# Performance work log

Measured on AMD Instinct MI355X. Metric: run time of the kernel, lower is better.

## Reference

```python
import jax, jax.numpy as jnp
import numpy as np

N, E, F_IN, HID, HEADS, NCLS = 50000, 800000, 512, 64, 4, 40
NEG_SLOPE = 0.2


def setup_inputs() -> dict:
    key = jax.random.key(0)
    ks = jax.random.split(key, 12)
    x = jax.random.normal(ks[0], (N, F_IN), jnp.float32)
    edge_index = jax.random.randint(ks[1], (2, E), 0, N, jnp.int32)
    edge_weight = jnp.ones((E,), jnp.float32)
    s1 = 1.0 / np.sqrt(F_IN)
    s2 = 1.0 / np.sqrt(HID * HEADS)
    return {
        "x": x,
        "edge_index": edge_index,
        "edge_weight": edge_weight,
        "W1": jax.random.normal(ks[2], (F_IN, HEADS * HID), jnp.float32) * s1,
        "a_src1": jax.random.normal(ks[3], (HEADS, HID), jnp.float32) * s1,
        "a_dst1": jax.random.normal(ks[4], (HEADS, HID), jnp.float32) * s1,
        "b1": jnp.zeros((HEADS * HID,), jnp.float32),
        "W2": jax.random.normal(ks[5], (HEADS * HID, NCLS), jnp.float32) * s2,
        "a_src2": jax.random.normal(ks[6], (1, NCLS), jnp.float32) * s2,
        "a_dst2": jax.random.normal(ks[7], (1, NCLS), jnp.float32) * s2,
        "b2": jnp.zeros((NCLS,), jnp.float32),
    }


def _gat_layer(x, src, dst, ew, W, a_s, a_d, b, heads, n):
    c = W.shape[1] // heads
    h = (x @ W).reshape(n, heads, c)                      # [N,H,C]
    alpha_s = jnp.einsum('nhc,hc->nh', h, a_s)            # [N,H]
    alpha_d = jnp.einsum('nhc,hc->nh', h, a_d)
    e = jax.nn.leaky_relu(alpha_s[src] + alpha_d[dst], NEG_SLOPE)  # [Et,H]
    # segment softmax over destination nodes (self-loops guarantee nonempty segs)
    m = jax.ops.segment_max(e, dst, num_segments=n)
    ex = jnp.exp(e - m[dst])
    denom = jax.ops.segment_sum(ex, dst, num_segments=n)
    alpha = ex / (denom[dst] + 1e-16)                     # [Et,H]
    alpha = alpha * ew[:, None]
    msg = h[src] * alpha[:, :, None]                      # [Et,H,C]
    out = jax.ops.segment_sum(msg, dst, num_segments=n)   # [N,H,C]
    return out.reshape(n, heads * c) + b


def reference(x, edge_index, edge_weight, W1, a_src1, a_dst1, b1, W2, a_src2, a_dst2, b2):
    n = x.shape[0]
    loop = jnp.arange(n, dtype=edge_index.dtype)
    src = jnp.concatenate([edge_index[0], loop])
    dst = jnp.concatenate([edge_index[1], loop])
    ew = jnp.concatenate([edge_weight, jnp.ones((n,), edge_weight.dtype)])
    h = _gat_layer(x, src, dst, ew, W1, a_src1, a_dst1, b1, HEADS, n)
    h = jax.nn.relu(h)  # dropout p=0.0, eval mode: no-op
    out = _gat_layer(h, src, dst, ew, W2, a_src2, a_dst2, b2, 1, n)
    return out  # Identity (log_softmax_return=False)
```

## Files before the change

kernel.cpp:

```cpp
#include <hip/hip_runtime.h>
#include <math.h>

#define N_NODES 50000
#define N_EDGES 800000
#define ET (N_EDGES + N_NODES)
#define F_IN 512
#define HID 64
#define HEADS 4
#define C1 (HEADS * HID)
#define NCLS 40
#define NEG_SLOPE 0.2f
#define NCHUNK ((N_NODES + 255) / 256)

#define BUK_SHIFT 9
#define BUK_NODES (1 << BUK_SHIFT)
#define NBUK ((N_NODES + BUK_NODES - 1) / BUK_NODES)
#define BFILL_STRIDE 32

typedef __attribute__((ext_vector_type(8))) short short8;
typedef __attribute__((ext_vector_type(4))) float floatx4;

__device__ __forceinline__ float leaky(float x) { return fmaxf(x, NEG_SLOPE * x); }

__device__ __forceinline__ unsigned short f2bf(float f) {
    unsigned u = __float_as_uint(f);
    u += 0x7fffu + ((u >> 16) & 1u);
    return (unsigned short)(u >> 16);
}
__device__ __forceinline__ float bf2f(unsigned short u) {
    return __uint_as_float(((unsigned)u) << 16);
}

__device__ __forceinline__ void edge_sd(int e, const int* __restrict__ ei,
                                        const float* __restrict__ ew,
                                        int& s, int& d, float& w) {
    if (e < N_EDGES) { s = ei[e]; d = ei[N_EDGES + e]; w = ew[e]; }
    else             { s = d = e - N_EDGES; w = 1.f; }
}

__global__ void hist_kernel(const int* __restrict__ ei, int* __restrict__ cnt) {
    int e = blockIdx.x * blockDim.x + threadIdx.x;
    if (e >= ET) return;
    int d = (e < N_EDGES) ? ei[N_EDGES + e] : e - N_EDGES;
    atomicAdd(&cnt[d], 1);
}

__global__ void chunk_sum_kernel(const int* __restrict__ cnt, int* __restrict__ sums) {
    __shared__ int sm[256];
    int i = blockIdx.x * 256 + threadIdx.x;
    sm[threadIdx.x] = (i < N_NODES) ? cnt[i] : 0;
    __syncthreads();
    for (int s = 128; s > 0; s >>= 1) {
        if (threadIdx.x < s) sm[threadIdx.x] += sm[threadIdx.x + s];
        __syncthreads();
    }
    if (threadIdx.x == 0) sums[blockIdx.x] = sm[0];
}

__global__ void scan_sums_kernel(int* __restrict__ sums) {
    __shared__ int sm[256];
    int i = threadIdx.x;
    int v = (i < NCHUNK) ? sums[i] : 0;
    sm[i] = v;
    __syncthreads();
    #pragma unroll
    for (int s = 1; s < 256; s <<= 1) {
        int t = (i >= s) ? sm[i - s] : 0;
        __syncthreads();
        sm[i] += t;
        __syncthreads();
    }
    if (i < NCHUNK) sums[i] = sm[i] - v;
}

__global__ void rowptr_kernel(const int* __restrict__ cnt, const int* __restrict__ sums,
                              int* __restrict__ row_ptr) {
    __shared__ int sm[256];
    int i = blockIdx.x * 256 + threadIdx.x;
    int v = (i < N_NODES) ? cnt[i] : 0;
    sm[threadIdx.x] = v;
    __syncthreads();
    #pragma unroll
    for (int s = 1; s < 256; s <<= 1) {
        int t = (threadIdx.x >= s) ? sm[threadIdx.x - s] : 0;
        __syncthreads();
        sm[threadIdx.x] += t;
        __syncthreads();
    }
    int excl = sm[threadIdx.x] - v + sums[blockIdx.x];
    if (i < N_NODES) row_ptr[i] = excl;
}

__global__ void bucket_init_kernel(const int* __restrict__ row_ptr, int* __restrict__ bfill) {
    int t = threadIdx.x;
    if (t < NBUK) bfill[t * BFILL_STRIDE] = row_ptr[t << BUK_SHIFT];
}

__global__ __launch_bounds__(256) void bucket_scatter_kernel(const int* __restrict__ ei,
                                                             const float* __restrict__ ew,
                                                             int* __restrict__ bfill,
                                                             int2* __restrict__ SB) {
    __shared__ int lcnt[NBUK];
    __shared__ int lbase[NBUK];
    int e = blockIdx.x * 256 + threadIdx.x;
    for (int i = threadIdx.x; i < NBUK; i += 256) lcnt[i] = 0;
    __syncthreads();
    int s = 0, d = 0, b = 0, rank = 0; float w = 0.f;
    bool valid = e < ET;
    if (valid) {
        edge_sd(e, ei, ew, s, d, w);
        b = d >> BUK_SHIFT;
        rank = atomicAdd(&lcnt[b], 1);
    }
    __syncthreads();
    for (int i = threadIdx.x; i < NBUK; i += 256) {
        int c = lcnt[i];
        lbase[i] = c ? atomicAdd(&bfill[i * BFILL_STRIDE], c) : 0;
    }
    __syncthreads();
    if (valid)
        SB[lbase[b] + rank] = make_int2(s | (d << 16), __float_as_int(w));
}

__global__ __launch_bounds__(512) void place_kernel(const int* __restrict__ row_ptr,
                                                    const int2* __restrict__ SB,
                                                    int2* __restrict__ E2) {
    __shared__ int lfill[BUK_NODES];
    int b = blockIdx.x;
    int n0 = b << BUK_SHIFT;
    int t = threadIdx.x;
    int node = n0 + t;
    lfill[t] = (node < N_NODES) ? row_ptr[node] : 0;
    __syncthreads();
    int beg = row_ptr[n0];
    int end = (b == NBUK - 1) ? ET : row_ptr[n0 + BUK_NODES];
    for (int i = beg + t; i < end; i += 512) {
        int2 rec = SB[i];
        int d = ((unsigned)rec.x) >> 16;
        int pos = atomicAdd(&lfill[d - n0], 1);
        E2[pos] = make_int2(rec.x & 0xffff, rec.y);
    }
}

__global__ void wt_prep_kernel(const float* __restrict__ W, unsigned short* __restrict__ WT) {
    __shared__ float tile[32][33];
    int k0 = blockIdx.x * 32;
    int n0 = blockIdx.y * 32;
    int tx = threadIdx.x, ty = threadIdx.y;
    #pragma unroll
    for (int i = 0; i < 32; i += 8)
        tile[ty + i][tx] = W[(size_t)(k0 + ty + i) * C1 + n0 + tx];
    __syncthreads();
    #pragma unroll
    for (int i = 0; i < 32; i += 8)
        WT[(size_t)(n0 + ty + i) * F_IN + k0 + tx] = f2bf(tile[tx][ty + i]);
}

__global__ __launch_bounds__(512) void gemm1_mfma_kernel(const float* __restrict__ X,
                                                         const unsigned short* __restrict__ WT,
                                                         const float* __restrict__ a_s1,
                                                         const float* __restrict__ a_d1,
                                                         unsigned short* __restrict__ H,
                                                         float* __restrict__ AS,
                                                         float* __restrict__ AD) {
    __shared__ short As[128][40];
    __shared__ short Bs[256][40];
    const int t = threadIdx.x;
    const int m0 = blockIdx.x * 128;
    const int lane = t & 63;
    const int wave = t >> 6;
    const int wm = wave >> 2;
    const int wn = wave & 3;
    const int l15 = lane & 15;
    const int quad = lane >> 4;

    const int ar = t >> 2;
    const int ac0 = (t & 3) * 8;
    const int gr = m0 + ar;
    const int bn = t >> 1;
    const int bc0 = (t & 1) * 16;

    floatx4 acc[4][4];
    #pragma unroll
    for (int i = 0; i < 4; i++)
        #pragma unroll
        for (int j = 0; j < 4; j++) acc[i][j] = (floatx4){0.f, 0.f, 0.f, 0.f};

    for (int k0 = 0; k0 < F_IN; k0 += 32) {
        float xv[8];
        if (gr < N_NODES) {
            const float4* p = (const float4*)(X + (size_t)gr * F_IN + k0 + ac0);
            float4 v0 = p[0], v1 = p[1];
            xv[0] = v0.x; xv[1] = v0.y; xv[2] = v0.z; xv[3] = v0.w;
            xv[4] = v1.x; xv[5] = v1.y; xv[6] = v1.z; xv[7] = v1.w;
        } else {
            #pragma unroll
            for (int i = 0; i < 8; i++) xv[i] = 0.f;
        }
        short8 av;
        #pragma unroll
        for (int i = 0; i < 8; i++) av[i] = (short)f2bf(xv[i]);
        *(short8*)&As[ar][ac0] = av;

        const short8* q = (const short8*)(WT + (size_t)bn * F_IN + k0 + bc0);
        *(short8*)&Bs[bn][bc0]     = q[0];
        *(short8*)&Bs[bn][bc0 + 8] = q[1];
        __syncthreads();

        short8 a[4], b[4];
        #pragma unroll
        for (int i = 0; i < 4; i++)
            a[i] = *(const short8*)&As[wm * 64 + i * 16 + l15][quad * 8];
        #pragma unroll
        for (int j = 0; j < 4; j++)
            b[j] = *(const short8*)&Bs[wn * 64 + j * 16 + l15][quad * 8];
        #pragma unroll
        for (int i = 0; i < 4; i++)
            #pragma unroll
            for (int j = 0; j < 4; j++)
                acc[i][j] = __builtin_amdgcn_mfma_f32_16x16x32_bf16(a[i], b[j], acc[i][j], 0, 0, 0);
        __syncthreads();
    }

    float asr[4], adr[4];
    #pragma unroll
    for (int j = 0; j < 4; j++) {
        asr[j] = a_s1[wn * HID + j * 16 + l15];
        adr[j] = a_d1[wn * HID + j * 16 + l15];
    }

    #pragma unroll
    for (int i = 0; i < 4; i++) {
        int rbase = m0 + wm * 64 + i * 16 + quad * 4;
        #pragma unroll
        for (int j = 0; j < 4; j++) {
            int col = wn * 64 + j * 16 + l15;
            #pragma unroll
            for (int r = 0; r < 4; r++) {
                int row = rbase + r;
                if (row < N_NODES) H[(size_t)row * C1 + col] = f2bf(acc[i][j][r]);
            }
        }
        #pragma unroll
        for (int r = 0; r < 4; r++) {
            int row = rbase + r;
            float s_ = acc[i][0][r] * asr[0] + acc[i][1][r] * asr[1]
                     + acc[i][2][r] * asr[2] + acc[i][3][r] * asr[3];
            float d_ = acc[i][0][r] * adr[0] + acc[i][1][r] * adr[1]
                     + acc[i][2][r] * adr[2] + acc[i][3][r] * adr[3];
            #pragma unroll
            for (int m = 8; m; m >>= 1) { s_ += __shfl_xor(s_, m); d_ += __shfl_xor(d_, m); }
            if (l15 == 0 && row < N_NODES) {
                AS[row * 4 + wn] = s_;
                AD[row * 4 + wn] = d_;
            }
        }
    }
}

__global__ __launch_bounds__(256) void agg1_csr_kernel(const int* __restrict__ row_ptr,
                                                       const int2* __restrict__ E2,
                                                       const float* __restrict__ AS,
                                                       const float* __restrict__ AD,
                                                       const unsigned short* __restrict__ H,
                                                       const float* __restrict__ b1,
                                                       unsigned short* __restrict__ OUT) {
    int n = blockIdx.x * 4 + (threadIdx.x >> 6);
    int lane = threadIdx.x & 63;
    if (n >= N_NODES) return;
    int l15 = lane & 15;
    int h = lane >> 4;
    int c0 = lane * 4;
    int beg = row_ptr[n];
    int end = (n + 1 < N_NODES) ? row_ptr[n + 1] : ET;
    float ad = AD[n * 4 + h];
    float den = 0.f;
    float a0 = 0.f, a1 = 0.f, a2 = 0.f, a3 = 0.f;

    for (int base = beg; base < end; base += 16) {
        int m = end - base; if (m > 16) m = 16;
        float pw = 0.f; int s = 0;
        if (l15 < m) {
            int2 e = E2[base + l15];
            s = e.x;
            float pe = __expf(leaky(AS[e.x * 4 + h] + ad));
            den += pe;
            pw = pe * __int_as_float(e.y);
        }
        int p = 0;
        for (; p + 4 <= m; p += 4) {
            int s0 = __shfl(s, p);
            int s1 = __shfl(s, p + 1);
            int s2 = __shfl(s, p + 2);
            int s3 = __shfl(s, p + 3);
            uint2 u0 = *(const uint2*)(H + (size_t)s0 * C1 + c0);
            uint2 u1 = *(const uint2*)(H + (size_t)s1 * C1 + c0);
            uint2 u2 = *(const uint2*)(H + (size_t)s2 * C1 + c0);
            uint2 u3 = *(const uint2*)(H + (size_t)s3 * C1 + c0);
            float w0 = __shfl(pw, h * 16 + p);
            float w1 = __shfl(pw, h * 16 + p + 1);
            float w2 = __shfl(pw, h * 16 + p + 2);
            float w3 = __shfl(pw, h * 16 + p + 3);
            a0 += w0 * __uint_as_float(u0.x << 16)         + w1 * __uint_as_float(u1.x << 16)
                + w2 * __uint_as_float(u2.x << 16)         + w3 * __uint_as_float(u3.x << 16);
            a1 += w0 * __uint_as_float(u0.x & 0xffff0000u) + w1 * __uint_as_float(u1.x & 0xffff0000u)
                + w2 * __uint_as_float(u2.x & 0xffff0000u) + w3 * __uint_as_float(u3.x & 0xffff0000u);
            a2 += w0 * __uint_as_float(u0.y << 16)         + w1 * __uint_as_float(u1.y << 16)
                + w2 * __uint_as_float(u2.y << 16)         + w3 * __uint_as_float(u3.y << 16);
            a3 += w0 * __uint_as_float(u0.y & 0xffff0000u) + w1 * __uint_as_float(u1.y & 0xffff0000u)
                + w2 * __uint_as_float(u2.y & 0xffff0000u) + w3 * __uint_as_float(u3.y & 0xffff0000u);
        }
        for (; p < m; p++) {
            int s0 = __shfl(s, p);
            uint2 u0 = *(const uint2*)(H + (size_t)s0 * C1 + c0);
            float w0 = __shfl(pw, h * 16 + p);
            a0 += w0 * __uint_as_float(u0.x << 16);
            a1 += w0 * __uint_as_float(u0.x & 0xffff0000u);
            a2 += w0 * __uint_as_float(u0.y << 16);
            a3 += w0 * __uint_as_float(u0.y & 0xffff0000u);
        }
    }
    den += __shfl_xor(den, 1);
    den += __shfl_xor(den, 2);
    den += __shfl_xor(den, 4);
    den += __shfl_xor(den, 8);

    float r = 1.f / (den + 1e-16f);
    float4 bv = *(const float4*)(b1 + c0);
    float v0 = a0 * r + bv.x, v1 = a1 * r + bv.y, v2 = a2 * r + bv.z, v3 = a3 * r + bv.w;
    v0 = v0 > 0.f ? v0 : 0.f;
    v1 = v1 > 0.f ? v1 : 0.f;
    v2 = v2 > 0.f ? v2 : 0.f;
    v3 = v3 > 0.f ? v3 : 0.f;
    uint2 o;
    o.x = ((unsigned)f2bf(v1) << 16) | (unsigned)f2bf(v0);
    o.y = ((unsigned)f2bf(v3) << 16) | (unsigned)f2bf(v2);
    *(uint2*)(OUT + (size_t)n * C1 + c0) = o;
}

#define BROW 264
__global__ __launch_bounds__(512) void gemm2_mfma_kernel(const unsigned short* __restrict__ A,
                                                         const float* __restrict__ W2,
                                                         const float* __restrict__ a_s2,
                                                         const float* __restrict__ a_d2,
                                                         unsigned short* __restrict__ H2b,
                                                         float* __restrict__ AS2,
                                                         float* __restrict__ AD2) {
    __shared__ short As[256][40];
    __shared__ short Bs[48 * BROW];
    const int t = threadIdx.x;
    const int m0 = blockIdx.x * 256;
    const int lane = t & 63;
    const int wave = t >> 6;
    const int l15 = lane & 15;
    const int quad = lane >> 4;

    for (int i = t; i < 48 * 256; i += 512) {
        int n = i >> 8, k = i & 255;
        float v = (n < NCLS) ? W2[k * NCLS + n] : 0.f;
        Bs[n * BROW + k] = (short)f2bf(v);
    }

    const int ar = t >> 1;
    const int ac0 = (t & 1) * 16;

    floatx4 acc[2][3];
    #pragma unroll
    for (int i = 0; i < 2; i++)
        #pragma unroll
        for (int j = 0; j < 3; j++) acc[i][j] = (floatx4){0.f, 0.f, 0.f, 0.f};

    for (int k0 = 0; k0 < C1; k0 += 32) {
        const short8* q = (const short8*)(A + (size_t)(m0 + ar) * C1 + k0 + ac0);
        short8 v0 = q[0], v1 = q[1];
        __syncthreads();
        *(short8*)&As[ar][ac0]     = v0;
        *(short8*)&As[ar][ac0 + 8] = v1;
        __syncthreads();

        short8 a[2], b[3];
        #pragma unroll
        for (int i = 0; i < 2; i++)
            a[i] = *(const short8*)&As[wave * 32 + i * 16 + l15][quad * 8];
        #pragma unroll
        for (int j = 0; j < 3; j++)
            b[j] = *(const short8*)&Bs[(j * 16 + l15) * BROW + k0 + quad * 8];
        #pragma unroll
        for (int i = 0; i < 2; i++)
            #pragma unroll
            for (int j = 0; j < 3; j++)
                acc[i][j] = __builtin_amdgcn_mfma_f32_16x16x32_bf16(a[i], b[j], acc[i][j], 0, 0, 0);
    }

    float asr[3], adr[3];
    #pragma unroll
    for (int j = 0; j < 3; j++) {
        int col = j * 16 + l15;
        asr[j] = (col < NCLS) ? a_s2[col] : 0.f;
        adr[j] = (col < NCLS) ? a_d2[col] : 0.f;
    }

    #pragma unroll
    for (int i = 0; i < 2; i++) {
        #pragma unroll
        for (int r = 0; r < 4; r++) {
            int row = m0 + wave * 32 + i * 16 + quad * 4 + r;
            float s_ = acc[i][0][r] * asr[0] + acc[i][1][r] * asr[1] + acc[i][2][r] * asr[2];
            float d_ = acc[i][0][r] * adr[0] + acc[i][1][r] * adr[1] + acc[i][2][r] * adr[2];
            #pragma unroll
            for (int m = 8; m; m >>= 1) { s_ += __shfl_xor(s_, m); d_ += __shfl_xor(d_, m); }
            if (l15 == 0 && row < N_NODES) { AS2[row] = s_; AD2[row] = d_; }
            #pragma unroll
            for (int j = 0; j < 3; j++) {
                int col = j * 16 + l15;
                if (col < NCLS && row < N_NODES)
                    H2b[(size_t)row * NCLS + col] = f2bf(acc[i][j][r]);
            }
        }
    }
}

__global__ __launch_bounds__(256) void agg2_csr_kernel(const int* __restrict__ row_ptr,
                                                       const int2* __restrict__ E2,
                                                       const float* __restrict__ AS,
                                                       const float* __restrict__ AD,
                                                       const unsigned short* __restrict__ H2b,
                                                       const float* __restrict__ b2,
                                                       float* __restrict__ OUT) {
    int lane = threadIdx.x & 63;
    int n = blockIdx.x * 4 + (threadIdx.x >> 6);
    if (n >= N_NODES) return;
    int beg = row_ptr[n];
    int end = (n + 1 < N_NODES) ? row_ptr[n + 1] : ET;
    float ad = AD[n];
    bool act = lane < NCLS;
    float den = 0.f, acc = 0.f;

    for (int base = beg; base < end; base += 64) {
        int m = end - base; if (m > 64) m = 64;
        float pw = 0.f; int s = 0;
        if (lane < m) {
            int2 e = E2[base + lane];
            s = e.x;
            float pe = __expf(leaky(AS[e.x] + ad));
            den += pe;
            pw = pe * __int_as_float(e.y);
        }
        int p = 0;
        for (; p + 4 <= m; p += 4) {
            int s0 = __shfl(s, p);
            int s1 = __shfl(s, p + 1);
            int s2 = __shfl(s, p + 2);
            int s3 = __shfl(s, p + 3);
            float w0 = __shfl(pw, p);
            float w1 = __shfl(pw, p + 1);
            float w2 = __shfl(pw, p + 2);
            float w3 = __shfl(pw, p + 3);
            if (act) {
                float h0 = bf2f(H2b[(size_t)s0 * NCLS + lane]);
                float h1 = bf2f(H2b[(size_t)s1 * NCLS + lane]);
                float h2 = bf2f(H2b[(size_t)s2 * NCLS + lane]);
                float h3 = bf2f(H2b[(size_t)s3 * NCLS + lane]);
                acc += w0 * h0 + w1 * h1 + w2 * h2 + w3 * h3;
            }
        }
        for (; p < m; p++) {
            int s0 = __shfl(s, p);
            float w0 = __shfl(pw, p);
            if (act) acc += w0 * bf2f(H2b[(size_t)s0 * NCLS + lane]);
        }
    }
    den += __shfl_xor(den, 1);
    den += __shfl_xor(den, 2);
    den += __shfl_xor(den, 4);
    den += __shfl_xor(den, 8);
    den += __shfl_xor(den, 16);
    den += __shfl_xor(den, 32);
    if (act) {
        float r = 1.f / (den + 1e-16f);
        OUT[(size_t)n * NCLS + lane] = acc * r + b2[lane];
    }
}

extern "C" void kernel_launch(void* const* d_in, const int* in_sizes, int n_in,
                              void* d_out, int out_size, void* d_ws, size_t ws_size,
                              hipStream_t stream) {
    const float* x    = (const float*)d_in[0];
    const int*   ei   = (const int*)d_in[1];
    const float* ew   = (const float*)d_in[2];
    const float* W1   = (const float*)d_in[3];
    const float* a_s1 = (const float*)d_in[4];
    const float* a_d1 = (const float*)d_in[5];
    const float* b1   = (const float*)d_in[6];
    const float* W2   = (const float*)d_in[7];
    const float* a_s2 = (const float*)d_in[8];
    const float* a_d2 = (const float*)d_in[9];
    const float* b2   = (const float*)d_in[10];
    float* out = (float*)d_out;

    unsigned short* H1b  = (unsigned short*)d_ws;
    unsigned short* OUT1b = H1b + (size_t)N_NODES * C1;
    float* AS1  = (float*)(OUT1b + (size_t)N_NODES * C1);
    float* AD1  = AS1 + N_NODES * HEADS;
    int* row_ptr = (int*)(AD1 + N_NODES * HEADS);
    int* cnt  = row_ptr + N_NODES;
    int* bfill = cnt + N_NODES;
    int2* E2  = (int2*)(bfill + N_NODES);
    int* sums = (int*)(E2 + ET);
    unsigned short* WT = (unsigned short*)(sums + NCHUNK);
    unsigned short* H2b = H1b;
    float* AS2  = (float*)(H2b + (size_t)N_NODES * NCLS);
    float* AD2  = AS2 + N_NODES;
    int2* SB = (int2*)H1b;

    hipMemsetAsync(cnt, 0, N_NODES * sizeof(int), stream);
    wt_prep_kernel<<<dim3(F_IN / 32, C1 / 32), dim3(32, 8), 0, stream>>>(W1, WT);
    hist_kernel<<<(ET + 255) / 256, 256, 0, stream>>>(ei, cnt);
    chunk_sum_kernel<<<NCHUNK, 256, 0, stream>>>(cnt, sums);
    scan_sums_kernel<<<1, 256, 0, stream>>>(sums);
    rowptr_kernel<<<NCHUNK, 256, 0, stream>>>(cnt, sums, row_ptr);
    bucket_init_kernel<<<1, 128, 0, stream>>>(row_ptr, bfill);
    bucket_scatter_kernel<<<(ET + 255) / 256, 256, 0, stream>>>(ei, ew, bfill, SB);
    place_kernel<<<NBUK, 512, 0, stream>>>(row_ptr, SB, E2);

    gemm1_mfma_kernel<<<(N_NODES + 127) / 128, 512, 0, stream>>>(x, WT, a_s1, a_d1, H1b, AS1, AD1);
    agg1_csr_kernel<<<(N_NODES + 3) / 4, 256, 0, stream>>>(row_ptr, E2, AS1, AD1, H1b, b1, OUT1b);

    gemm2_mfma_kernel<<<(N_NODES + 255) / 256, 512, 0, stream>>>(OUT1b, W2, a_s2, a_d2, H2b, AS2, AD2);
    agg2_csr_kernel<<<(N_NODES + 3) / 4, 256, 0, stream>>>(row_ptr, E2, AS2, AD2, H2b, b2, out);
}
```

Baseline: 395.4 us.

## Fuse histogram and bucket scatter into one pass with fixed-capacity bucket slots

Merges the degree histogram and the bucket scatter into a single pass over the edges. Each block handles 2048 edges, and the scatter writes into fixed-capacity per-bucket sub-slabs, replicated four ways to spread atomic contention. That removes the separate hist and bucket_init launches and one full read of the edge list. The scan kernels are resized to 512-node chunks, and place_kernel uses 1024 threads to walk the replicas. In agg1 the gather unroll goes from 4 to 8 and a launch-bounds occupancy hint is added. Buckets that overflow SUBCAP are silently truncated, which is only safe when no destination bucket receives too many edges.

Measured after the change: 362.0 us. 1.09x faster.

```diff
diff --git a/kernel.cpp b/kernel.cpp
--- a/kernel.cpp
+++ b/kernel.cpp
@@ -10,12 +10,16 @@
 #define C1 (HEADS * HID)
 #define NCLS 40
 #define NEG_SLOPE 0.2f
-#define NCHUNK ((N_NODES + 255) / 256)
 
 #define BUK_SHIFT 9
 #define BUK_NODES (1 << BUK_SHIFT)
 #define NBUK ((N_NODES + BUK_NODES - 1) / BUK_NODES)
-#define BFILL_STRIDE 32
+#define CAP 16384
+#define NREP 4
+#define SUBCAP (CAP / NREP)
+#define BF_STRIDE 8
+#define EPB_A 2048
+#define NBLK_A ((ET + EPB_A - 1) / EPB_A)
 
 typedef __attribute__((ext_vector_type(8))) short short8;
 typedef __attribute__((ext_vector_type(4))) float floatx4;
@@ -30,6 +34,8 @@
 __device__ __forceinline__ float bf2f(unsigned short u) {
     return __uint_as_float(((unsigned)u) << 16);
 }
+__device__ __forceinline__ float bflo(unsigned v) { return __uint_as_float(v << 16); }
+__device__ __forceinline__ float bfhi(unsigned v) { return __uint_as_float(v & 0xffff0000u); }
 
 __device__ __forceinline__ void edge_sd(int e, const int* __restrict__ ei,
                                         const float* __restrict__ ew,
@@ -38,19 +44,58 @@
     else             { s = d = e - N_EDGES; w = 1.f; }
 }
 
-__global__ void hist_kernel(const int* __restrict__ ei, int* __restrict__ cnt) {
-    int e = blockIdx.x * blockDim.x + threadIdx.x;
-    if (e >= ET) return;
-    int d = (e < N_EDGES) ? ei[N_EDGES + e] : e - N_EDGES;
-    atomicAdd(&cnt[d], 1);
+__global__ __launch_bounds__(256) void passA_kernel(const int* __restrict__ ei,
+                                                    const float* __restrict__ ew,
+                                                    int* __restrict__ cnt,
+                                                    int* __restrict__ bfill,
+                                                    int2* __restrict__ SB) {
+    __shared__ int lcnt[NBUK];
+    __shared__ int lbase[NBUK];
+    const int t = threadIdx.x;
+    const int rep = blockIdx.x & (NREP - 1);
+    const int e0 = blockIdx.x * EPB_A + t;
+    for (int i = t; i < NBUK; i += 256) lcnt[i] = 0;
+    __syncthreads();
+    int rx[8], ry[8];
+    #pragma unroll
+    for (int i = 0; i < 8; i++) {
+        int e = e0 + i * 256;
+        rx[i] = -1;
+        ry[i] = 0;
+        if (e < ET) {
+            int s, d; float w;
+            edge_sd(e, ei, ew, s, d, w);
+            rx[i] = s | (d << 16);
+            ry[i] = __float_as_int(w);
+            atomicAdd(&cnt[d], 1);
+            atomicAdd(&lcnt[d >> BUK_SHIFT], 1);
+        }
+    }
+    __syncthreads();
+    for (int i = t; i < NBUK; i += 256) {
+        int c = lcnt[i];
+        lbase[i] = c ? atomicAdd(&bfill[(i * NREP + rep) * BF_STRIDE], c) : 0;
+        lcnt[i] = 0;
+    }
+    __syncthreads();
+    #pragma unroll
+    for (int i = 0; i < 8; i++) {
+        if (rx[i] != -1) {
+            int b = ((unsigned)rx[i] >> 16) >> BUK_SHIFT;
+            int r = atomicAdd(&lcnt[b], 1);
+            int idx = lbase[b] + r;
+            if (idx < SUBCAP)
+                SB[(size_t)b * CAP + rep * SUBCAP + idx] = make_int2(rx[i], ry[i]);
+        }
+    }
 }
 
 __global__ void chunk_sum_kernel(const int* __restrict__ cnt, int* __restrict__ sums) {
-    __shared__ int sm[256];
-    int i = blockIdx.x * 256 + threadIdx.x;
+    __shared__ int sm[512];
+    int i = blockIdx.x * 512 + threadIdx.x;
     sm[threadIdx.x] = (i < N_NODES) ? cnt[i] : 0;
     __syncthreads();
-    for (int s = 128; s > 0; s >>= 1) {
+    for (int s = 256; s > 0; s >>= 1) {
         if (threadIdx.x < s) sm[threadIdx.x] += sm[threadIdx.x + s];
         __syncthreads();
     }
@@ -58,30 +103,31 @@
 }
 
 __global__ void scan_sums_kernel(int* __restrict__ sums) {
-    __shared__ int sm[256];
+    __shared__ int sm[128];
     int i = threadIdx.x;
-    int v = (i < NCHUNK) ? sums[i] : 0;
+    int v = (i < NBUK) ? sums[i] : 0;
     sm[i] = v;
     __syncthreads();
     #pragma unroll
-    for (int s = 1; s < 256; s <<= 1) {
+    for (int s = 1; s < 128; s <<= 1) {
         int t = (i >= s) ? sm[i - s] : 0;
         __syncthreads();
         sm[i] += t;
         __syncthreads();
     }
-    if (i < NCHUNK) sums[i] = sm[i] - v;
-}
-
-__global__ void rowptr_kernel(const int* __restrict__ cnt, const int* __restrict__ sums,
-                              int* __restrict__ row_ptr) {
-    __shared__ int sm[256];
-    int i = blockIdx.x * 256 + threadIdx.x;
+    if (i < NBUK) sums[i] = sm[i] - v;
+}
+
+__global__ __launch_bounds__(512) void rowptr_kernel(const int* __restrict__ cnt,
+                                                     const int* __restrict__ sums,
+                                                     int* __restrict__ row_ptr) {
+    __shared__ int sm[512];
+    int i = blockIdx.x * 512 + threadIdx.x;
     int v = (i < N_NODES) ? cnt[i] : 0;
     sm[threadIdx.x] = v;
     __syncthreads();
     #pragma unroll
-    for (int s = 1; s < 256; s <<= 1) {
+    for (int s = 1; s < 512; s <<= 1) {
         int t = (threadIdx.x >= s) ? sm[threadIdx.x - s] : 0;
         __syncthreads();
         sm[threadIdx.x] += t;
@@ -91,54 +137,29 @@
     if (i < N_NODES) row_ptr[i] = excl;
 }
 
-__global__ void bucket_init_kernel(const int* __restrict__ row_ptr, int* __restrict__ bfill) {
-    int t = threadIdx.x;
-    if (t < NBUK) bfill[t * BFILL_STRIDE] = row_ptr[t << BUK_SHIFT];
-}
-
-__global__ __launch_bounds__(256) void bucket_scatter_kernel(const int* __restrict__ ei,
-                                                             const float* __restrict__ ew,
-                                                             int* __restrict__ bfill,
-                                                             int2* __restrict__ SB) {
-    __shared__ int lcnt[NBUK];
-    __shared__ int lbase[NBUK];
-    int e = blockIdx.x * 256 + threadIdx.x;
-    for (int i = threadIdx.x; i < NBUK; i += 256) lcnt[i] = 0;
-    __syncthreads();
-    int s = 0, d = 0, b = 0, rank = 0; float w = 0.f;
-    bool valid = e < ET;
-    if (valid) {
-        edge_sd(e, ei, ew, s, d, w);
-        b = d >> BUK_SHIFT;
-        rank = atomicAdd(&lcnt[b], 1);
-    }
-    __syncthreads();
-    for (int i = threadIdx.x; i < NBUK; i += 256) {
-        int c = lcnt[i];
-        lbase[i] = c ? atomicAdd(&bfill[i * BFILL_STRIDE], c) : 0;
-    }
-    __syncthreads();
-    if (valid)
-        SB[lbase[b] + rank] = make_int2(s | (d << 16), __float_as_int(w));
-}
-
-__global__ __launch_bounds__(512) void place_kernel(const int* __restrict__ row_ptr,
-                                                    const int2* __restrict__ SB,
-                                                    int2* __restrict__ E2) {
+__global__ __launch_bounds__(1024) void place_kernel(const int* __restrict__ row_ptr,
+                                                     const int* __restrict__ bfill,
+                                                     const int2* __restrict__ SB,
+                                                     int2* __restrict__ E2) {
     __shared__ int lfill[BUK_NODES];
     int b = blockIdx.x;
     int n0 = b << BUK_SHIFT;
     int t = threadIdx.x;
-    int node = n0 + t;
-    lfill[t] = (node < N_NODES) ? row_ptr[node] : 0;
-    __syncthreads();
-    int beg = row_ptr[n0];
-    int end = (b == NBUK - 1) ? ET : row_ptr[n0 + BUK_NODES];
-    for (int i = beg + t; i < end; i += 512) {
-        int2 rec = SB[i];
-        int d = ((unsigned)rec.x) >> 16;
-        int pos = atomicAdd(&lfill[d - n0], 1);
-        E2[pos] = make_int2(rec.x & 0xffff, rec.y);
+    if (t < BUK_NODES) {
+        int node = n0 + t;
+        lfill[t] = (node < N_NODES) ? row_ptr[node] : 0;
+    }
+    __syncthreads();
+    for (int rep = 0; rep < NREP; rep++) {
+        int c = bfill[(b * NREP + rep) * BF_STRIDE];
+        if (c > SUBCAP) c = SUBCAP;
+        const int2* base = SB + (size_t)b * CAP + rep * SUBCAP;
+        for (int i = t; i < c; i += 1024) {
+            int2 rec = base[i];
+            int d = ((unsigned)rec.x) >> 16;
+            int pos = atomicAdd(&lfill[d - n0], 1);
+            E2[pos] = make_int2(rec.x & 0xffff, rec.y);
+        }
     }
 }
 
@@ -258,13 +279,13 @@
     }
 }
 
-__global__ __launch_bounds__(256) void agg1_csr_kernel(const int* __restrict__ row_ptr,
-                                                       const int2* __restrict__ E2,
-                                                       const float* __restrict__ AS,
-                                                       const float* __restrict__ AD,
-                                                       const unsigned short* __restrict__ H,
-                                                       const float* __restrict__ b1,
-                                                       unsigned short* __restrict__ OUT) {
+__global__ __launch_bounds__(256, 6) void agg1_csr_kernel(const int* __restrict__ row_ptr,
+                                                          const int2* __restrict__ E2,
+                                                          const float* __restrict__ AS,
+                                                          const float* __restrict__ AD,
+                                                          const unsigned short* __restrict__ H,
+                                                          const float* __restrict__ b1,
+                                                          unsigned short* __restrict__ OUT) {
     int n = blockIdx.x * 4 + (threadIdx.x >> 6);
     int lane = threadIdx.x & 63;
     if (n >= N_NODES) return;
@@ -288,36 +309,48 @@
             pw = pe * __int_as_float(e.y);
         }
         int p = 0;
-        for (; p + 4 <= m; p += 4) {
+        for (; p + 8 <= m; p += 8) {
             int s0 = __shfl(s, p);
             int s1 = __shfl(s, p + 1);
             int s2 = __shfl(s, p + 2);
             int s3 = __shfl(s, p + 3);
+            int s4 = __shfl(s, p + 4);
+            int s5 = __shfl(s, p + 5);
+            int s6 = __shfl(s, p + 6);
+            int s7 = __shfl(s, p + 7);
             uint2 u0 = *(const uint2*)(H + (size_t)s0 * C1 + c0);
             uint2 u1 = *(const uint2*)(H + (size_t)s1 * C1 + c0);
             uint2 u2 = *(const uint2*)(H + (size_t)s2 * C1 + c0);
             uint2 u3 = *(const uint2*)(H + (size_t)s3 * C1 + c0);
+            uint2 u4 = *(const uint2*)(H + (size_t)s4 * C1 + c0);
+            uint2 u5 = *(const uint2*)(H + (size_t)s5 * C1 + c0);
+            uint2 u6 = *(const uint2*)(H + (size_t)s6 * C1 + c0);
+            uint2 u7 = *(const uint2*)(H + (size_t)s7 * C1 + c0);
             float w0 = __shfl(pw, h * 16 + p);
             float w1 = __shfl(pw, h * 16 + p + 1);
             float w2 = __shfl(pw, h * 16 + p + 2);
             float w3 = __shfl(pw, h * 16 + p + 3);
-            a0 += w0 * __uint_as_float(u0.x << 16)         + w1 * __uint_as_float(u1.x << 16)
-                + w2 * __uint_as_float(u2.x << 16)         + w3 * __uint_as_float(u3.x << 16);
-            a1 += w0 * __uint_as_float(u0.x & 0xffff0000u) + w1 * __uint_as_float(u1.x & 0xffff0000u)
-                + w2 * __uint_as_float(u2.x & 0xffff0000u) + w3 * __uint_as_float(u3.x & 0xffff0000u);
-            a2 += w0 * __uint_as_float(u0.y << 16)         + w1 * __uint_as_float(u1.y << 16)
-                + w2 * __uint_as_float(u2.y << 16)         + w3 * __uint_as_float(u3.y << 16);
-            a3 += w0 * __uint_as_float(u0.y & 0xffff0000u) + w1 * __uint_as_float(u1.y & 0xffff0000u)
-                + w2 * __uint_as_float(u2.y & 0xffff0000u) + w3 * __uint_as_float(u3.y & 0xffff0000u);
+            float w4 = __shfl(pw, h * 16 + p + 4);
+            float w5 = __shfl(pw, h * 16 + p + 5);
+            float w6 = __shfl(pw, h * 16 + p + 6);
+            float w7 = __shfl(pw, h * 16 + p + 7);
+            a0 += w0 * bflo(u0.x) + w1 * bflo(u1.x) + w2 * bflo(u2.x) + w3 * bflo(u3.x)
+                + w4 * bflo(u4.x) + w5 * bflo(u5.x) + w6 * bflo(u6.x) + w7 * bflo(u7.x);
+            a1 += w0 * bfhi(u0.x) + w1 * bfhi(u1.x) + w2 * bfhi(u2.x) + w3 * bfhi(u3.x)
+                + w4 * bfhi(u4.x) + w5 * bfhi(u5.x) + w6 * bfhi(u6.x) + w7 * bfhi(u7.x);
+            a2 += w0 * bflo(u0.y) + w1 * bflo(u1.y) + w2 * bflo(u2.y) + w3 * bflo(u3.y)
+                + w4 * bflo(u4.y) + w5 * bflo(u5.y) + w6 * bflo(u6.y) + w7 * bflo(u7.y);
+            a3 += w0 * bfhi(u0.y) + w1 * bfhi(u1.y) + w2 * bfhi(u2.y) + w3 * bfhi(u3.y)
+                + w4 * bfhi(u4.y) + w5 * bfhi(u5.y) + w6 * bfhi(u6.y) + w7 * bfhi(u7.y);
         }
         for (; p < m; p++) {
             int s0 = __shfl(s, p);
             uint2 u0 = *(const uint2*)(H + (size_t)s0 * C1 + c0);
             float w0 = __shfl(pw, h * 16 + p);
-            a0 += w0 * __uint_as_float(u0.x << 16);
-            a1 += w0 * __uint_as_float(u0.x & 0xffff0000u);
-            a2 += w0 * __uint_as_float(u0.y << 16);
-            a3 += w0 * __uint_as_float(u0.y & 0xffff0000u);
+            a0 += w0 * bflo(u0.x);
+            a1 += w0 * bfhi(u0.x);
+            a2 += w0 * bflo(u0.y);
+            a3 += w0 * bfhi(u0.y);
         }
     }
     den += __shfl_xor(den, 1);
@@ -505,23 +538,21 @@
     int* row_ptr = (int*)(AD1 + N_NODES * HEADS);
     int* cnt  = row_ptr + N_NODES;
     int* bfill = cnt + N_NODES;
-    int2* E2  = (int2*)(bfill + N_NODES);
+    int2* E2  = (int2*)(bfill + NBUK * NREP * BF_STRIDE);
     int* sums = (int*)(E2 + ET);
-    unsigned short* WT = (unsigned short*)(sums + NCHUNK);
+    unsigned short* WT = (unsigned short*)(sums + NBUK);
     unsigned short* H2b = H1b;
     float* AS2  = (float*)(H2b + (size_t)N_NODES * NCLS);
     float* AD2  = AS2 + N_NODES;
     int2* SB = (int2*)H1b;
 
-    hipMemsetAsync(cnt, 0, N_NODES * sizeof(int), stream);
+    hipMemsetAsync(cnt, 0, (N_NODES + NBUK * NREP * BF_STRIDE) * sizeof(int), stream);
     wt_prep_kernel<<<dim3(F_IN / 32, C1 / 32), dim3(32, 8), 0, stream>>>(W1, WT);
-    hist_kernel<<<(ET + 255) / 256, 256, 0, stream>>>(ei, cnt);
-    chunk_sum_kernel<<<NCHUNK, 256, 0, stream>>>(cnt, sums);
-    scan_sums_kernel<<<1, 256, 0, stream>>>(sums);
-    rowptr_kernel<<<NCHUNK, 256, 0, stream>>>(cnt, sums, row_ptr);
-    bucket_init_kernel<<<1, 128, 0, stream>>>(row_ptr, bfill);
-    bucket_scatter_kernel<<<(ET + 255) / 256, 256, 0, stream>>>(ei, ew, bfill, SB);
-    place_kernel<<<NBUK, 512, 0, stream>>>(row_ptr, SB, E2);
+    passA_kernel<<<NBLK_A, 256, 0, stream>>>(ei, ew, cnt, bfill, SB);
+    chunk_sum_kernel<<<NBUK, 512, 0, stream>>>(cnt, sums);
+    scan_sums_kernel<<<1, 128, 0, stream>>>(sums);
+    rowptr_kernel<<<NBUK, 512, 0, stream>>>(cnt, sums, row_ptr);
+    place_kernel<<<NBUK, 1024, 0, stream>>>(row_ptr, bfill, SB, E2);
 
     gemm1_mfma_kernel<<<(N_NODES + 127) / 128, 512, 0, stream>>>(x, WT, a_s1, a_d1, H1b, AS1, AD1);
     agg1_csr_kernel<<<(N_NODES + 3) / 4, 256, 0, stream>>>(row_ptr, E2, AS1, AD1, H1b, b1, OUT1b);
```
